# Performance work log

Hardware: AMD Instinct MI355X
Metric: run time of the kernel (lower is better)

## Reference

```python
import jax, jax.numpy as jnp
import numpy as np

RES = 512       # grid resolution per plane
NFEAT = 32      # features per plane level
LRELU_SLOPE = 0.2
PLANE_AXES = ((0, 1), (0, 2), (1, 2))  # NPlaneSum: xy, xz, yz planes


def encode_nplanesum(x_t, planes):
    """x_t: [N,3] in [0,1]; planes: [3,RES,RES,NFEAT]. Bilinear interp on 3 planes, summed."""
    pos = x_t * (RES - 1)                      # [N,3]
    p0f = jnp.floor(pos)
    frac = pos - p0f                           # [N,3]
    p0 = jnp.clip(p0f.astype(jnp.int32), 0, RES - 1)
    p1 = jnp.minimum(p0 + 1, RES - 1)
    h = jnp.zeros((x_t.shape[0], NFEAT), dtype=planes.dtype)
    for k, (a, b) in enumerate(PLANE_AXES):
        pl = planes[k]                         # [RES,RES,NFEAT]
        i0, i1 = p0[:, a], p1[:, a]
        j0, j1 = p0[:, b], p1[:, b]
        fa = frac[:, a:a + 1]
        fb = frac[:, b:b + 1]
        v00 = pl[i0, j0]; v01 = pl[i0, j1]
        v10 = pl[i1, j0]; v11 = pl[i1, j1]
        h = h + (v00 * (1 - fb) + v01 * fb) * (1 - fa) + (v10 * (1 - fb) + v11 * fb) * fa
    return h


def decode_fp16(h, W1, b1, W2, b2):
    """Tiny MLP run in fp16 (as in Decoder), equal_lr scaling = 1/sqrt(fan_in)."""
    s = np.float16(1.0 / np.sqrt(NFEAT))
    y = h.astype(jnp.float16)
    y = jnp.dot(y, W1.astype(jnp.float16) * s) + b1.astype(jnp.float16)
    y = jnp.where(y >= 0, y, jnp.float16(LRELU_SLOPE) * y)   # LeakyReLU(0.2)
    y = jnp.dot(y, W2.astype(jnp.float16) * s) + b2.astype(jnp.float16)
    return y.astype(jnp.float32)                             # [N,4]


def setup_inputs() -> dict:
    key = jax.random.key(0)
    k1, k2, k3, k4 = jax.random.split(key, 4)
    N = 2_097_152
    x = jax.random.uniform(k1, (N, 3), dtype=jnp.float32, minval=-1.0, maxval=1.0)
    planes = jax.random.normal(k2, (3, RES, RES, NFEAT), dtype=jnp.float32) * 0.05
    W1 = jax.random.normal(k3, (NFEAT, NFEAT), dtype=jnp.float32)
    b1 = jnp.zeros((NFEAT,), dtype=jnp.float32)
    W2 = jax.random.normal(k4, (NFEAT, 4), dtype=jnp.float32)
    b2 = jnp.zeros((4,), dtype=jnp.float32)
    return {"x": x, "planes": planes, "W1": W1, "b1": b1, "W2": W2, "b2": b2}


def reference(x, planes, W1, b1, W2, b2):
    # transform_points is identity (K=None); map [-1,1] -> [0,1]
    x_t = (x + 1.0) * 0.5
    h = encode_nplanesum(x_t, planes)
    out = decode_fp16(h, W1, b1, W2, b2)           # [N,4]
    sdf = out[..., 0]
    rgb = (jnp.tanh(out[..., 1:]) + 1.0) * 0.5
    # analytic normals: d(sdf)/d(x_t), matching forward_sdf_nablas
    sdf_sum = lambda xt: decode_fp16(encode_nplanesum(xt, planes), W1, b1, W2, b2)[..., 0].sum()
    nablas = jax.grad(sdf_sum)(x_t)                # [N,3]
    return sdf, h, nablas, rgb
```

## Files before the change

### kernel.cpp

```cpp
#include <hip/hip_runtime.h>
#include <hip/hip_fp16.h>

#define RES 512
#define NF 32

typedef float v2f __attribute__((ext_vector_type(2)));

static __device__ __forceinline__ float h2f(float v) {
    return __half2float(__float2half(v));
}
static __device__ __forceinline__ v2f mkv2(float a, float b) { v2f r; r.x = a; r.y = b; return r; }

template <int L>
static __device__ __forceinline__ float qb(float v) {
    return __int_as_float(__builtin_amdgcn_mov_dpp(
        __float_as_int(v), (L | (L << 2) | (L << 4) | (L << 6)), 0xf, 0xf, true));
}
static __device__ __forceinline__ float qsum(float v) {
    v += __int_as_float(__builtin_amdgcn_mov_dpp(__float_as_int(v), 0xB1, 0xf, 0xf, true));
    v += __int_as_float(__builtin_amdgcn_mov_dpp(__float_as_int(v), 0x4E, 0xf, 0xf, true));
    return v;
}

#define GET(v, c) ((c) == 0 ? (v).x : ((c) == 1 ? (v).y : ((c) == 2 ? (v).z : (v).w)))

__global__ __launch_bounds__(256) void stylesdf_fused(
    const float* __restrict__ x,
    const float* __restrict__ planes,
    const float* __restrict__ W1,
    const float* __restrict__ b1,
    const float* __restrict__ W2,
    const float* __restrict__ b2,
    float* __restrict__ out, int N)
{
#pragma clang fp contract(off)
    __shared__ __align__(16) float sW1[NF * NF];
    __shared__ __align__(16) float sW1T[NF * NF];
    __shared__ __align__(16) float sW2[NF * 4];
    __shared__ __align__(16) float sB1[NF];
    __shared__ __align__(16) float sB2[4];
    __shared__ __align__(16) float sW2c0[NF];

    const float S16 = h2f(0.17677669529663687f);
    const float LREL = h2f(0.2f);

    const int tid = threadIdx.x;
    for (int idx = tid; idx < NF * NF; idx += 256) {
        float w = h2f(h2f(W1[idx]) * S16);
        sW1[idx] = w;
        sW1T[(idx & 31) * NF + (idx >> 5)] = w;
    }
    if (tid < NF * 4) sW2[tid] = h2f(h2f(W2[tid]) * S16);
    if (tid < NF) { sB1[tid] = h2f(b1[tid]); sW2c0[tid] = h2f(h2f(W2[tid * 4]) * S16); }
    if (tid < 4) sB2[tid] = h2f(b2[tid]);
    __syncthreads();

    const int gt = blockIdx.x * 256 + tid;
    const int p = gt >> 2;
    if (p >= N) return;
    const int q = gt & 3;
    const int fq = q << 2;

    float fr0, fr1, fr2;
    int a0lo, a0hi, a1lo, a1hi, a2lo, a2hi;
#define AXIS(c, FR, LO, HI)                                 \
    {                                                       \
        float xt = (x[3 * p + (c)] + 1.0f) * 0.5f;          \
        float pos = xt * 511.0f;                            \
        float pf = floorf(pos);                             \
        FR = pos - pf;                                      \
        int qq = (int)pf;                                   \
        qq = qq < 0 ? 0 : (qq > 511 ? 511 : qq);            \
        LO = qq;                                            \
        HI = (qq + 1 > 511) ? 511 : qq + 1;                 \
    }
    AXIS(0, fr0, a0lo, a0hi)
    AXIS(1, fr1, a1lo, a1hi)
    AXIS(2, fr2, a2lo, a2hi)
#undef AXIS

    const int oA00 = (a0lo * RES + a1lo) << 5, oA01 = (a0lo * RES + a1hi) << 5;
    const int oA10 = (a0hi * RES + a1lo) << 5, oA11 = (a0hi * RES + a1hi) << 5;
    const int oB00 = (a0lo * RES + a2lo) << 5, oB01 = (a0lo * RES + a2hi) << 5;
    const int oB10 = (a0hi * RES + a2lo) << 5, oB11 = (a0hi * RES + a2hi) << 5;
    const int oC00 = (a1lo * RES + a2lo) << 5, oC01 = (a1lo * RES + a2hi) << 5;
    const int oC10 = (a1hi * RES + a2lo) << 5, oC11 = (a1hi * RES + a2hi) << 5;
    const float* pl0 = planes;
    const float* pl1 = planes + RES * RES * NF;
    const float* pl2 = planes + 2 * (RES * RES * NF);

#define LD4(b, off) (*(const float4*)((b) + (off)))

    const float ifa01 = 1.0f - fr0, ifb01 = 1.0f - fr1;
    const float ifa02 = 1.0f - fr0, ifb02 = 1.0f - fr2;
    const float ifa12 = 1.0f - fr1, ifb12 = 1.0f - fr2;

    float hl[8];
    float d0l[8], d1l[8], d2l[8];
    float4* ho = (float4*)(out + (size_t)N + (size_t)p * NF);

#pragma unroll
    for (int kk = 0; kk < 2; ++kk) {
        const int fo = fq + 16 * kk;
        const float4 vA00 = LD4(pl0, oA00 + fo), vA01 = LD4(pl0, oA01 + fo);
        const float4 vA10 = LD4(pl0, oA10 + fo), vA11 = LD4(pl0, oA11 + fo);
        const float4 vB00 = LD4(pl1, oB00 + fo), vB01 = LD4(pl1, oB01 + fo);
        const float4 vB10 = LD4(pl1, oB10 + fo), vB11 = LD4(pl1, oB11 + fo);
        const float4 vC00 = LD4(pl2, oC00 + fo), vC01 = LD4(pl2, oC01 + fo);
        const float4 vC10 = LD4(pl2, oC10 + fo), vC11 = LD4(pl2, oC11 + fo);
        float hc[4];
#pragma unroll
        for (int c = 0; c < 4; ++c) {
            const int f = 4 * kk + c;
            {
                const float a00 = GET(vA00, c), a01 = GET(vA01, c);
                const float a10 = GET(vA10, c), a11 = GET(vA11, c);
                const float t4 = (a00 * ifb01 + a01 * fr1) * ifa01;
                const float t8 = (a10 * ifb01 + a11 * fr1) * fr0;
                hc[c] = t4 + t8;
                d0l[f] = (a10 - a00) * ifb01 + (a11 - a01) * fr1;
                d1l[f] = (a01 - a00) * ifa01 + (a11 - a10) * fr0;
            }
            {
                const float a00 = GET(vB00, c), a01 = GET(vB01, c);
                const float a10 = GET(vB10, c), a11 = GET(vB11, c);
                const float t4 = (a00 * ifb02 + a01 * fr2) * ifa02;
                const float t8 = (a10 * ifb02 + a11 * fr2) * fr0;
                hc[c] = (hc[c] + t4) + t8;
                d0l[f] += (a10 - a00) * ifb02 + (a11 - a01) * fr2;
                d2l[f] = (a01 - a00) * ifa02 + (a11 - a10) * fr0;
            }
            {
                const float a00 = GET(vC00, c), a01 = GET(vC01, c);
                const float a10 = GET(vC10, c), a11 = GET(vC11, c);
                const float t4 = (a00 * ifb12 + a01 * fr2) * ifa12;
                const float t8 = (a10 * ifb12 + a11 * fr2) * fr1;
                hc[c] = (hc[c] + t4) + t8;
                d1l[f] += (a10 - a00) * ifb12 + (a11 - a01) * fr2;
                d2l[f] += (a01 - a00) * ifa12 + (a11 - a10) * fr1;
            }
            hl[f] = h2f(hc[c]);
        }
        ho[q + 4 * kk] = make_float4(hc[0], hc[1], hc[2], hc[3]);
    }

    v2f y2[4];
    y2[0] = mkv2(0.f, 0.f); y2[1] = mkv2(0.f, 0.f);
    y2[2] = mkv2(0.f, 0.f); y2[3] = mkv2(0.f, 0.f);

#define YSTEP(half, ow, e)                                                     \
    {                                                                          \
        const int i = 16 * (half) + 4 * (ow) + (e);                            \
        const float hi = qb<(ow)>(hl[(e) + 4 * (half)]);                       \
        const v2f hv = mkv2(hi, hi);                                           \
        const float4 wA = *(const float4*)(sW1 + i * NF + fq);                 \
        const float4 wB = *(const float4*)(sW1 + i * NF + fq + 16);            \
        y2[0] = y2[0] + hv * mkv2(wA.x, wA.y);       \
        y2[1] = y2[1] + hv * mkv2(wA.z, wA.w);                                 \
        y2[2] = y2[2] + hv * mkv2(wB.x, wB.y);                                 \
        y2[3] = y2[3] + hv * mkv2(wB.z, wB.w);                                 \
    }
#define Y4(half, ow) YSTEP(half, ow, 0) YSTEP(half, ow, 1) YSTEP(half, ow, 2) YSTEP(half, ow, 3)
#define Y16(half) Y4(half, 0) Y4(half, 1) Y4(half, 2) Y4(half, 3)
    Y16(0) Y16(1)
#undef Y16
#undef Y4
#undef YSTEP

    float o0 = 0.f, o1 = 0.f, o2 = 0.f, o3 = 0.f;
    float ml[8];
#pragma unroll
    for (int t = 0; t < 8; ++t) {
        const int j = fq + (t & 3) + 16 * (t >> 2);
        const float yt = (t & 1) ? y2[t >> 1].y : y2[t >> 1].x;
        const float yd = h2f(yt);
        const float y16 = h2f(yd + sB1[j]);
        const bool nn = y16 >= 0.0f;
        const float zj = nn ? y16 : h2f(LREL * y16);
        const float4 w2 = ((const float4*)sW2)[j];
        o0 = o0 + zj * w2.x;
        o1 = o1 + zj * w2.y;
        o2 = o2 + zj * w2.z;
        o3 = o3 + zj * w2.w;
        ml[t] = (nn ? 1.0f : LREL) * sW2c0[j];
    }

    v2f g2[4];
    g2[0] = mkv2(0.f, 0.f); g2[1] = mkv2(0.f, 0.f);
    g2[2] = mkv2(0.f, 0.f); g2[3] = mkv2(0.f, 0.f);

#define GSTEP(half, ow, e)                                                     \
    {                                                                          \
        const int j = 16 * (half) + 4 * (ow) + (e);                            \
        const float mj = qb<(ow)>(ml[(e) + 4 * (half)]);                       \
        const v2f mv = mkv2(mj, mj);                                           \
        const float4 wA = *(const float4*)(sW1T + j * NF + fq);                \
        const float4 wB = *(const float4*)(sW1T + j * NF + fq + 16);           \
        g2[0] = __builtin_elementwise_fma(mv, mkv2(wA.x, wA.y), g2[0]);        \
        g2[1] = __builtin_elementwise_fma(mv, mkv2(wA.z, wA.w), g2[1]);        \
        g2[2] = __builtin_elementwise_fma(mv, mkv2(wB.x, wB.y), g2[2]);        \
        g2[3] = __builtin_elementwise_fma(mv, mkv2(wB.z, wB.w), g2[3]);        \
    }
#define G4(half, ow) GSTEP(half, ow, 0) GSTEP(half, ow, 1) GSTEP(half, ow, 2) GSTEP(half, ow, 3)
#define G16(half) G4(half, 0) G4(half, 1) G4(half, 2) G4(half, 3)
    G16(0) G16(1)
#undef G16
#undef G4
#undef GSTEP

    float n0 = 0.f, n1 = 0.f, n2 = 0.f;
#pragma unroll
    for (int t = 0; t < 8; ++t) {
        const float gt_ = (t & 1) ? g2[t >> 1].y : g2[t >> 1].x;
        n0 = fmaf(gt_, d0l[t], n0);
        n1 = fmaf(gt_, d1l[t], n1);
        n2 = fmaf(gt_, d2l[t], n2);
    }

    o0 = qsum(o0); o1 = qsum(o1); o2 = qsum(o2); o3 = qsum(o3);
    n0 = qsum(n0); n1 = qsum(n1); n2 = qsum(n2);

    o0 = h2f(h2f(o0) + sB2[0]);
    o1 = h2f(h2f(o1) + sB2[1]);
    o2 = h2f(h2f(o2) + sB2[2]);
    o3 = h2f(h2f(o3) + sB2[3]);
    n0 *= 511.0f; n1 *= 511.0f; n2 *= 511.0f;

    if (q == 0) out[p] = o0;
    if (q == 1) {
        const size_t nb = (size_t)N * 33 + (size_t)p * 3;
        out[nb + 0] = n0; out[nb + 1] = n1; out[nb + 2] = n2;
    }
    if (q == 2) {
        const size_t rb = (size_t)N * 36 + (size_t)p * 3;
        out[rb + 0] = (tanhf(o1) + 1.0f) * 0.5f;
        out[rb + 1] = (tanhf(o2) + 1.0f) * 0.5f;
        out[rb + 2] = (tanhf(o3) + 1.0f) * 0.5f;
    }
#undef LD4
#undef GET
}

extern "C" void kernel_launch(void* const* d_in, const int* in_sizes, int n_in,
                              void* d_out, int out_size, void* d_ws, size_t ws_size,
                              hipStream_t stream) {
    const float* x      = (const float*)d_in[0];
    const float* planes = (const float*)d_in[1];
    const float* W1     = (const float*)d_in[2];
    const float* b1     = (const float*)d_in[3];
    const float* W2     = (const float*)d_in[4];
    const float* b2     = (const float*)d_in[5];
    float* out = (float*)d_out;
    const int N = in_sizes[0] / 3;
    const long long total = 4LL * N;
    const int blocks = (int)((total + 255) / 256);
    stylesdf_fused<<<blocks, 256, 0, stream>>>(x, planes, W1, b1, W2, b2, out, N);
}
```

Before: 918.5 us.

## Compute normals via forward-mode tangents sharing W1 loads, drop transposed W1

Result: faster. 888.9 us (-3.2%).

```diff
diff --git a/kernel.cpp b/kernel.cpp
--- a/kernel.cpp
+++ b/kernel.cpp
@@ -35,7 +35,6 @@
 {
 #pragma clang fp contract(off)
     __shared__ __align__(16) float sW1[NF * NF];
-    __shared__ __align__(16) float sW1T[NF * NF];
     __shared__ __align__(16) float sW2[NF * 4];
     __shared__ __align__(16) float sB1[NF];
     __shared__ __align__(16) float sB2[4];
@@ -45,11 +44,8 @@
     const float LREL = h2f(0.2f);
 
     const int tid = threadIdx.x;
-    for (int idx = tid; idx < NF * NF; idx += 256) {
-        float w = h2f(h2f(W1[idx]) * S16);
-        sW1[idx] = w;
-        sW1T[(idx & 31) * NF + (idx >> 5)] = w;
-    }
+    for (int idx = tid; idx < NF * NF; idx += 256)
+        sW1[idx] = h2f(h2f(W1[idx]) * S16);
     if (tid < NF * 4) sW2[tid] = h2f(h2f(W2[tid]) * S16);
     if (tid < NF) { sB1[tid] = h2f(b1[tid]); sW2c0[tid] = h2f(h2f(W2[tid * 4]) * S16); }
     if (tid < 4) sB2[tid] = h2f(b2[tid]);
@@ -144,21 +140,43 @@
         ho[q + 4 * kk] = make_float4(hc[0], hc[1], hc[2], hc[3]);
     }
 
-    v2f y2[4];
-    y2[0] = mkv2(0.f, 0.f); y2[1] = mkv2(0.f, 0.f);
-    y2[2] = mkv2(0.f, 0.f); y2[3] = mkv2(0.f, 0.f);
-
-#define YSTEP(half, ow, e)                                                     \
+    v2f y2[4], e0v[4], e1v[4], e2v[4];
+#pragma unroll
+    for (int k = 0; k < 4; ++k) {
+        y2[k] = mkv2(0.f, 0.f);
+        e0v[k] = mkv2(0.f, 0.f); e1v[k] = mkv2(0.f, 0.f); e2v[k] = mkv2(0.f, 0.f);
+    }
+
+#define YSTEP(half, ow, e_)                                                    \
     {                                                                          \
-        const int i = 16 * (half) + 4 * (ow) + (e);                            \
-        const float hi = qb<(ow)>(hl[(e) + 4 * (half)]);                       \
+        const int i_ = 16 * (half) + 4 * (ow) + (e_);                          \
+        const int t_ = (e_) + 4 * (half);                                      \
+        const float hi = qb<(ow)>(hl[t_]);                                     \
+        const float dA = qb<(ow)>(d0l[t_]);                                    \
+        const float dB = qb<(ow)>(d1l[t_]);                                    \
+        const float dC = qb<(ow)>(d2l[t_]);                                    \
+        const float4 wA = *(const float4*)(sW1 + i_ * NF + fq);                \
+        const float4 wB = *(const float4*)(sW1 + i_ * NF + fq + 16);           \
+        const v2f w0 = mkv2(wA.x, wA.y), w1 = mkv2(wA.z, wA.w);                \
+        const v2f w2v = mkv2(wB.x, wB.y), w3 = mkv2(wB.z, wB.w);               \
         const v2f hv = mkv2(hi, hi);                                           \
-        const float4 wA = *(const float4*)(sW1 + i * NF + fq);                 \
-        const float4 wB = *(const float4*)(sW1 + i * NF + fq + 16);            \
-        y2[0] = y2[0] + hv * mkv2(wA.x, wA.y);       \
-        y2[1] = y2[1] + hv * mkv2(wA.z, wA.w);                                 \
-        y2[2] = y2[2] + hv * mkv2(wB.x, wB.y);                                 \
-        y2[3] = y2[3] + hv * mkv2(wB.z, wB.w);                                 \
+        y2[0] = y2[0] + hv * w0;      \
+        y2[1] = y2[1] + hv * w1;                                               \
+        y2[2] = y2[2] + hv * w2v;                                              \
+        y2[3] = y2[3] + hv * w3;                                               \
+        const v2f av = mkv2(dA, dA), bv = mkv2(dB, dB), cv = mkv2(dC, dC);     \
+        e0v[0] = __builtin_elementwise_fma(av, w0, e0v[0]);                    \
+        e0v[1] = __builtin_elementwise_fma(av, w1, e0v[1]);                    \
+        e0v[2] = __builtin_elementwise_fma(av, w2v, e0v[2]);                   \
+        e0v[3] = __builtin_elementwise_fma(av, w3, e0v[3]);                    \
+        e1v[0] = __builtin_elementwise_fma(bv, w0, e1v[0]);                    \
+        e1v[1] = __builtin_elementwise_fma(bv, w1, e1v[1]);                    \
+        e1v[2] = __builtin_elementwise_fma(bv, w2v, e1v[2]);                   \
+        e1v[3] = __builtin_elementwise_fma(bv, w3, e1v[3]);                    \
+        e2v[0] = __builtin_elementwise_fma(cv, w0, e2v[0]);                    \
+        e2v[1] = __builtin_elementwise_fma(cv, w1, e2v[1]);                    \
+        e2v[2] = __builtin_elementwise_fma(cv, w2v, e2v[2]);                   \
+        e2v[3] = __builtin_elementwise_fma(cv, w3, e2v[3]);                    \
     }
 #define Y4(half, ow) YSTEP(half, ow, 0) YSTEP(half, ow, 1) YSTEP(half, ow, 2) YSTEP(half, ow, 3)
 #define Y16(half) Y4(half, 0) Y4(half, 1) Y4(half, 2) Y4(half, 3)
@@ -168,7 +186,7 @@
 #undef YSTEP
 
     float o0 = 0.f, o1 = 0.f, o2 = 0.f, o3 = 0.f;
-    float ml[8];
+    float n0 = 0.f, n1 = 0.f, n2 = 0.f;
 #pragma unroll
     for (int t = 0; t < 8; ++t) {
         const int j = fq + (t & 3) + 16 * (t >> 2);
@@ -182,39 +200,13 @@
         o1 = o1 + zj * w2.y;
         o2 = o2 + zj * w2.z;
         o3 = o3 + zj * w2.w;
-        ml[t] = (nn ? 1.0f : LREL) * sW2c0[j];
-    }
-
-    v2f g2[4];
-    g2[0] = mkv2(0.f, 0.f); g2[1] = mkv2(0.f, 0.f);
-    g2[2] = mkv2(0.f, 0.f); g2[3] = mkv2(0.f, 0.f);
-
-#define GSTEP(half, ow, e)                                                     \
-    {                                                                          \
-        const int j = 16 * (half) + 4 * (ow) + (e);                            \
-        const float mj = qb<(ow)>(ml[(e) + 4 * (half)]);                       \
-        const v2f mv = mkv2(mj, mj);                                           \
-        const float4 wA = *(const float4*)(sW1T + j * NF + fq);                \
-        const float4 wB = *(const float4*)(sW1T + j * NF + fq + 16);           \
-        g2[0] = __builtin_elementwise_fma(mv, mkv2(wA.x, wA.y), g2[0]);        \
-        g2[1] = __builtin_elementwise_fma(mv, mkv2(wA.z, wA.w), g2[1]);        \
-        g2[2] = __builtin_elementwise_fma(mv, mkv2(wB.x, wB.y), g2[2]);        \
-        g2[3] = __builtin_elementwise_fma(mv, mkv2(wB.z, wB.w), g2[3]);        \
-    }
-#define G4(half, ow) GSTEP(half, ow, 0) GSTEP(half, ow, 1) GSTEP(half, ow, 2) GSTEP(half, ow, 3)
-#define G16(half) G4(half, 0) G4(half, 1) G4(half, 2) G4(half, 3)
-    G16(0) G16(1)
-#undef G16
-#undef G4
-#undef GSTEP
-
-    float n0 = 0.f, n1 = 0.f, n2 = 0.f;
-#pragma unroll
-    for (int t = 0; t < 8; ++t) {
-        const float gt_ = (t & 1) ? g2[t >> 1].y : g2[t >> 1].x;
-        n0 = fmaf(gt_, d0l[t], n0);
-        n1 = fmaf(gt_, d1l[t], n1);
-        n2 = fmaf(gt_, d2l[t], n2);
+        const float mj = (nn ? 1.0f : LREL) * sW2c0[j];
+        const float ea = (t & 1) ? e0v[t >> 1].y : e0v[t >> 1].x;
+        const float eb = (t & 1) ? e1v[t >> 1].y : e1v[t >> 1].x;
+        const float ec = (t & 1) ? e2v[t >> 1].y : e2v[t >> 1].x;
+        n0 = fmaf(mj, ea, n0);
+        n1 = fmaf(mj, eb, n1);
+        n2 = fmaf(mj, ec, n2);
     }
 
     o0 = qsum(o0); o1 = qsum(o1); o2 = qsum(o2); o3 = qsum(o3);
```
